# Performance work log

Hardware: AMD Instinct MI355X
Metric: run time of the kernel (lower is better)

Reference implementation:

```python
import jax, jax.numpy as jnp
import numpy as np
import math

D_MODEL = 1024
NUM_HEADS = 16
D_K = 64
B, T = 2, 2048


def setup_inputs() -> dict:
    key = jax.random.key(0)
    ks = jax.random.split(key, 12)
    s = 0.02
    return {
        "Q": jax.random.normal(ks[0], (B, T, D_MODEL), jnp.float32),
        "K": jax.random.normal(ks[1], (B, T, D_MODEL), jnp.float32),
        "V": jax.random.normal(ks[2], (B, T, D_MODEL), jnp.float32),
        # stacked per-head projection weights: [H, d_model, d_k]
        "Wq": jax.random.normal(ks[3], (NUM_HEADS, D_MODEL, D_K), jnp.float32) * s,
        "bq": jax.random.normal(ks[4], (NUM_HEADS, D_K), jnp.float32) * s,
        "Wk": jax.random.normal(ks[5], (NUM_HEADS, D_MODEL, D_K), jnp.float32) * s,
        "bk": jax.random.normal(ks[6], (NUM_HEADS, D_K), jnp.float32) * s,
        "Wv": jax.random.normal(ks[7], (NUM_HEADS, D_MODEL, D_K), jnp.float32) * s,
        "bv": jax.random.normal(ks[8], (NUM_HEADS, D_K), jnp.float32) * s,
        "Wo": jax.random.normal(ks[9], (D_MODEL, D_MODEL), jnp.float32) * s,
        "bo": jax.random.normal(ks[10], (D_MODEL,), jnp.float32) * s,
    }


def reference(Q, K, V, Wq, bq, Wk, bk, Wv, bv, Wo, bo):
    scale = 1.0 / math.sqrt(D_K)
    # fused batched per-head projections (replaces the Python per-head loop)
    Qh = jnp.einsum("btd,hdk->bhtk", Q, Wq) + bq[None, :, None, :]
    Kh = jnp.einsum("btd,hdk->bhtk", K, Wk) + bk[None, :, None, :]
    Vh = jnp.einsum("btd,hdk->bhtk", V, Wv) + bv[None, :, None, :]
    scores = jnp.einsum("bhtk,bhsk->bhts", Qh, Kh) * scale  # [B,H,T,T]
    attn = jax.nn.softmax(scores, axis=-1)
    ctx = jnp.einsum("bhts,bhsk->bhtk", attn, Vh)  # [B,H,T,d_k]
    # Faithful to the original: plain view of contiguous [B,H,T,d] into
    # [B,T,H*d] WITHOUT transposing head/time (matches torch .view semantics).
    bsz, nt = Q.shape[0], Q.shape[1]
    x = ctx.reshape(bsz, nt, NUM_HEADS * D_K)
    out = x @ Wo.T + bo
    # dropout with p=0.0 is identity; omitted for determinism
    return out
```

## Files before the change

### kernel.cpp

```cpp
#include <hip/hip_runtime.h>
#include <stdint.h>

typedef __attribute__((ext_vector_type(8))) short short8;
typedef __attribute__((ext_vector_type(4))) short short4v;
typedef __attribute__((ext_vector_type(4))) float float4v;

#define MFMA16(a, b, c) __builtin_amdgcn_mfma_f32_16x16x32_bf16((a), (b), (c), 0, 0, 0)

__device__ __forceinline__ ushort f2bf_rne(float f) {
  union { float f; unsigned u; } x; x.f = f;
  unsigned r = x.u + 0x7FFFu + ((x.u >> 16) & 1u);
  return (ushort)(r >> 16);
}
__device__ __forceinline__ ushort f2bf_trunc(float f) {
  union { float f; unsigned u; } x; x.f = f;
  return (ushort)(x.u >> 16);
}
__device__ __forceinline__ void gload16(const ushort* g, ushort* lds) {
  __builtin_amdgcn_global_load_lds(
      (__attribute__((address_space(1))) unsigned int*)g,
      (__attribute__((address_space(3))) unsigned int*)lds, 16, 0, 0);
}

#define CEXP 0.1803368801111204f

__device__ __forceinline__ void transpose64f(const float* __restrict__ in, int is,
                                             ushort* __restrict__ out, int os,
                                             ushort* lds ) {
  const int t = threadIdx.x;
#pragma unroll
  for (int it = 0; it < 2; ++it) {
    int e = it * 2048 + t * 8;
    int r = e >> 6, c = e & 63;
    const float* p = in + (size_t)r * is + c;
    float4 x0 = *(const float4*)p;
    float4 x1 = *(const float4*)(p + 4);
    ushort tv[8] __attribute__((aligned(16))) = {
        f2bf_rne(x0.x), f2bf_rne(x0.y), f2bf_rne(x0.z), f2bf_rne(x0.w),
        f2bf_rne(x1.x), f2bf_rne(x1.y), f2bf_rne(x1.z), f2bf_rne(x1.w)};
    *(uint4*)&lds[r * 72 + c] = *(const uint4*)tv;
  }
  __syncthreads();
  const int cc = t >> 2;
  const int rg = (t & 3) * 16;
  ushort tmp[16] __attribute__((aligned(16)));
#pragma unroll
  for (int i = 0; i < 16; ++i) tmp[i] = lds[(rg + i) * 72 + cc];
  *(uint4*)&out[(size_t)cc * os + rg] = *(const uint4*)&tmp[0];
  *(uint4*)&out[(size_t)cc * os + rg + 8] = *(const uint4*)&tmp[8];
}

__global__ __launch_bounds__(256) void prep_kernel(
    const float* __restrict__ Q, const float* __restrict__ K,
    const float* __restrict__ V, const float* __restrict__ Wo,
    const float* __restrict__ Wq, const float* __restrict__ Wk,
    const float* __restrict__ Wv, ushort* __restrict__ Qb, ushort* __restrict__ Kb,
    ushort* __restrict__ Vb, ushort* __restrict__ WoB, ushort* __restrict__ BtQ,
    ushort* __restrict__ BtK, ushort* __restrict__ BtV) {
  __shared__ ushort lds[64 * 72];
  const int bx = blockIdx.x;
  if (bx < 6656) {
    const float* s;
    ushort* d;
    int i;
    if (bx < 6144) {
      const int plane = bx >> 11;
      s = plane == 0 ? Q : (plane == 1 ? K : V);
      d = plane == 0 ? Qb : (plane == 1 ? Kb : Vb);
      i = ((bx & 2047) * 256 + threadIdx.x) * 8;
    } else {
      s = Wo;
      d = WoB;
      i = ((bx - 6144) * 256 + threadIdx.x) * 8;
    }
    float4 a = *(const float4*)(s + i);
    float4 b = *(const float4*)(s + i + 4);
    ushort t[8] __attribute__((aligned(16))) = {
        f2bf_rne(a.x), f2bf_rne(a.y), f2bf_rne(a.z), f2bf_rne(a.w),
        f2bf_rne(b.x), f2bf_rne(b.y), f2bf_rne(b.z), f2bf_rne(b.w)};
    *(uint4*)(d + i) = *(const uint4*)t;
  } else {
    const int rb = bx - 6656;
    const int dt = rb & 15, h = (rb >> 4) & 15, z = rb >> 8;
    const float* W = z == 0 ? Wq : (z == 1 ? Wk : Wv);
    ushort* Bt = z == 0 ? BtQ : (z == 1 ? BtK : BtV);
    transpose64f(W + h * 65536 + dt * 4096, 64, Bt + h * 65536 + dt * 64, 1024, lds);
  }
}

__global__ __launch_bounds__(256, 2) void repack_w_kernel(
    const float* __restrict__ Wq, const float* __restrict__ Wk,
    const float* __restrict__ Wv, ushort* __restrict__ BtQ, ushort* __restrict__ BtK,
    ushort* __restrict__ BtV) {
  __shared__ ushort lds[64 * 72];
  const float* W = blockIdx.z == 0 ? Wq : (blockIdx.z == 1 ? Wk : Wv);
  ushort* Bt = blockIdx.z == 0 ? BtQ : (blockIdx.z == 1 ? BtK : BtV);
  const int h = blockIdx.y, dt = blockIdx.x;
  transpose64f(W + h * 65536 + dt * 4096, 64, Bt + h * 65536 + dt * 64, 1024, lds);
}

template <int F32>
__device__ __forceinline__ void stage16(const void* G, size_t eoff, ushort* ldst) {
  if (F32) {
    const float* p = (const float*)G + eoff;
    float4 x0 = *(const float4*)p;
    float4 x1 = *(const float4*)(p + 4);
    ushort t[8] __attribute__((aligned(16))) = {
        f2bf_rne(x0.x), f2bf_rne(x0.y), f2bf_rne(x0.z), f2bf_rne(x0.w),
        f2bf_rne(x1.x), f2bf_rne(x1.y), f2bf_rne(x1.z), f2bf_rne(x1.w)};
    *(uint4*)ldst = *(const uint4*)t;
  } else {
    gload16((const ushort*)G + eoff, ldst);
  }
}

template <int AF32, int BF32>
__device__ __forceinline__ void gemm_body_basic(const void* __restrict__ A,
                                                const void* __restrict__ Bt,
                                                const float* __restrict__ bias,
                                                void* __restrict__ C, int cmode,
                                                float ascale, int N, int K, ushort* lA,
                                                ushort* lB) {
  const int tid = threadIdx.x;
  const int l = tid & 63, lane15 = l & 15, quad = l >> 4;
  const int mbase = blockIdx.y * 128, nbase = blockIdx.x * 128;
  const int w = tid >> 6;
  const int wrow = (w >> 1) * 64, wcol = (w & 1) * 64;
  const int e0 = tid * 8;
  const int e1 = 2048 + tid * 8;
  const int r0 = e0 >> 5, c0 = e0 & 31;
  const int r1 = e1 >> 5, c1 = e1 & 31;

  float4v acc[4][4];
#pragma unroll
  for (int i = 0; i < 4; ++i)
#pragma unroll
    for (int j = 0; j < 4; ++j) acc[i][j] = (float4v){0.f, 0.f, 0.f, 0.f};

  for (int kb = 0; kb < K; kb += 32) {
    __syncthreads();
    stage16<AF32>(A, (size_t)(mbase + r0) * K + c0 + kb, &lA[e0]);
    stage16<AF32>(A, (size_t)(mbase + r1) * K + c1 + kb, &lA[e1]);
    stage16<BF32>(Bt, (size_t)(nbase + r0) * K + c0 + kb, &lB[e0]);
    stage16<BF32>(Bt, (size_t)(nbase + r1) * K + c1 + kb, &lB[e1]);
    asm volatile("s_waitcnt vmcnt(0)" ::: "memory");
    __syncthreads();
    short8 a[4], b[4];
#pragma unroll
    for (int i = 0; i < 4; ++i) {
      a[i] = *(const short8*)&lA[(wrow + i * 16 + lane15) * 32 + quad * 8];
      b[i] = *(const short8*)&lB[(wcol + i * 16 + lane15) * 32 + quad * 8];
    }
#pragma unroll
    for (int i = 0; i < 4; ++i)
#pragma unroll
      for (int j = 0; j < 4; ++j) acc[i][j] = MFMA16(a[i], b[j], acc[i][j]);
  }

  if (cmode == 3) {
    __syncthreads();
    uint* sp = (uint*)lA + w * 576;
    const int bb = mbase >> 11;
    const int tb = (mbase & 2047) + wrow;
#pragma unroll
    for (int j = 0; j < 4; ++j) {
      {
        const int n = nbase + wcol + j * 16 + lane15;
        const float bvs = bias[n];
#pragma unroll
        for (int i = 0; i < 4; ++i)
#pragma unroll
          for (int rp = 0; rp < 2; ++rp) {
            const uint lo = f2bf_rne((acc[i][j][2 * rp] + bvs) * ascale);
            const uint hi = f2bf_rne((acc[i][j][2 * rp + 1] + bvs) * ascale);
            sp[36 * lane15 + i * 8 + quad * 2 + rp] = lo | (hi << 16);
          }
      }
#pragma unroll
      for (int t = 0; t < 2; ++t) {
        const int row = t * 8 + (l >> 3);
        const int c = l & 7;
        uint4 d = *(const uint4*)(sp + 36 * row + 4 * c);
        const int ng = nbase + wcol + j * 16 + row;
        ushort* dst = (ushort*)C + ((size_t)(bb * 1024 + ng)) * 2048 + tb + c * 8;
        *(uint4*)dst = d;
      }
    }
    return;
  }

#pragma unroll
  for (int j = 0; j < 4; ++j) {
    const int n = nbase + wcol + j * 16 + lane15;
    const float bvs = bias[n];
#pragma unroll
    for (int i = 0; i < 4; ++i) {
      const int m0 = mbase + wrow + i * 16 + quad * 4;
#pragma unroll
      for (int r = 0; r < 4; ++r) {
        const float val = (acc[i][j][r] + bvs) * ascale;
        if (cmode == 1) {
          const int m = m0 + r;
          const int bb = m >> 11, t = m & 2047;
          ((ushort*)C)[((size_t)(bb * 1024 + n)) * 2048 + t] = f2bf_rne(val);
        } else if (cmode == 2) {
          ((float*)C)[(size_t)(m0 + r) * N + n] = val;
        } else {
          ((ushort*)C)[(size_t)(m0 + r) * N + n] = f2bf_rne(val);
        }
      }
    }
  }
}

__global__ __launch_bounds__(256, 2) void proj3_kernel(
    const ushort* __restrict__ Qb, const ushort* __restrict__ Kb,
    const ushort* __restrict__ Vb, const ushort* __restrict__ BtQ,
    const ushort* __restrict__ BtK, const ushort* __restrict__ BtV,
    const float* __restrict__ bq, const float* __restrict__ bk,
    const float* __restrict__ bv, ushort* __restrict__ Qh, ushort* __restrict__ Kh,
    ushort* __restrict__ Vt) {
  __shared__ ushort lA[5120], lB[4096];
  if (blockIdx.z == 0)
    gemm_body_basic<0, 0>(Qb, BtQ, bq, Qh, 0, CEXP, 1024, 1024, lA, lB);
  else if (blockIdx.z == 1)
    gemm_body_basic<0, 0>(Kb, BtK, bk, Kh, 0, 1.0f, 1024, 1024, lA, lB);
  else
    gemm_body_basic<0, 0>(Vb, BtV, bv, Vt, 3, 1.0f, 1024, 1024, lA, lB);
}

__global__ __launch_bounds__(256, 2) void gemm_out_kernel(
    const ushort* __restrict__ X, const ushort* __restrict__ WoB,
    const float* __restrict__ bo, float* __restrict__ out) {
  __shared__ ushort lA[4096], lB[2048];
  const int tid = threadIdx.x;
  const int l = tid & 63, lane15 = l & 15, quad = l >> 4;
  const int mbase = blockIdx.y * 128, nbase = blockIdx.x * 64;
  const int wv = tid >> 6;
  const int wrow = wv * 32;
  const int e0 = tid * 8;
  const int e1 = 2048 + tid * 8;
  const int r0 = e0 >> 5, c0 = e0 & 31;
  const int r1 = e1 >> 5, c1 = e1 & 31;
  const ushort* Ag0 = X + (size_t)(mbase + r0) * 1024 + c0;
  const ushort* Ag1 = X + (size_t)(mbase + r1) * 1024 + c1;
  const ushort* Bg0 = WoB + (size_t)(nbase + r0) * 1024 + c0;

  float4v acc[2][4];
#pragma unroll
  for (int i = 0; i < 2; ++i)
#pragma unroll
    for (int j = 0; j < 4; ++j) acc[i][j] = (float4v){0.f, 0.f, 0.f, 0.f};

  for (int kb = 0; kb < 1024; kb += 32) {
    __syncthreads();
    gload16(Ag0 + kb, &lA[e0]);
    gload16(Ag1 + kb, &lA[e1]);
    gload16(Bg0 + kb, &lB[e0]);
    asm volatile("s_waitcnt vmcnt(0)" ::: "memory");
    __syncthreads();
    short8 a[2], b[4];
#pragma unroll
    for (int i = 0; i < 2; ++i)
      a[i] = *(const short8*)&lA[(wrow + i * 16 + lane15) * 32 + quad * 8];
#pragma unroll
    for (int j = 0; j < 4; ++j)
      b[j] = *(const short8*)&lB[(j * 16 + lane15) * 32 + quad * 8];
#pragma unroll
    for (int i = 0; i < 2; ++i)
#pragma unroll
      for (int j = 0; j < 4; ++j) acc[i][j] = MFMA16(a[i], b[j], acc[i][j]);
  }

#pragma unroll
  for (int j = 0; j < 4; ++j) {
    const int n = nbase + j * 16 + lane15;
    const float bvs = bo[n];
#pragma unroll
    for (int i = 0; i < 2; ++i) {
      const int m0 = mbase + wrow + i * 16 + quad * 4;
#pragma unroll
      for (int r = 0; r < 4; ++r) out[(size_t)(m0 + r) * 1024 + n] = acc[i][j][r] + bvs;
    }
  }
}

__global__ __launch_bounds__(256, 2) void proj3f_kernel(
    const float* __restrict__ Q, const float* __restrict__ Kin,
    const float* __restrict__ V, const ushort* __restrict__ BtQ,
    const ushort* __restrict__ BtK, const ushort* __restrict__ BtV,
    const float* __restrict__ bq, const float* __restrict__ bk,
    const float* __restrict__ bv, ushort* __restrict__ Qh, ushort* __restrict__ Kh,
    ushort* __restrict__ Vt) {
  __shared__ ushort lA[5120], lB[4096];
  if (blockIdx.z == 0)
    gemm_body_basic<1, 0>(Q, BtQ, bq, Qh, 0, CEXP, 1024, 1024, lA, lB);
  else if (blockIdx.z == 1)
    gemm_body_basic<1, 0>(Kin, BtK, bk, Kh, 0, 1.0f, 1024, 1024, lA, lB);
  else
    gemm_body_basic<1, 0>(V, BtV, bv, Vt, 3, 1.0f, 1024, 1024, lA, lB);
}

__global__ __launch_bounds__(256, 2) void gemm_btf_kernel(
    const ushort* __restrict__ X, const float* __restrict__ Wo,
    const float* __restrict__ bo, float* __restrict__ out) {
  __shared__ ushort lA[5120], lB[4096];
  gemm_body_basic<0, 1>(X, Wo, bo, out, 2, 1.0f, 1024, 1024, lA, lB);
}

__global__ __launch_bounds__(512, 4) void attn_kernel(const ushort* __restrict__ Qh,
                                                      const ushort* __restrict__ Kh,
                                                      const ushort* __restrict__ Vt,
                                                      ushort* __restrict__ ctxout) {
  __shared__ ushort lK[2][64 * 64];
  __shared__ ushort lV[2][64 * 64];
  __shared__ ushort pl_all[8][16 * 68];
  const int tid = threadIdx.x, l = tid & 63, wv = tid >> 6;
  const int lane15 = l & 15, quad = l >> 4;
  const int bh = blockIdx.x, b = bh >> 4, h = bh & 15;
  const int q0 = blockIdx.y * 128 + wv * 16;

  const int sr = tid >> 3;
  const int scb = (tid & 7) ^ (sr & 7);
  const ushort* Kp = Kh + (size_t)(b * 2048) * 1024 + h * 64;
  const ushort* Vp = Vt + (size_t)(bh * 64) * 2048;
  const ushort* Kg = Kp + (size_t)sr * 1024 + scb * 8;
  const ushort* Vg = Vp + (size_t)sr * 2048 + scb * 8;

  const ushort* qrow = Qh + (size_t)(b * 2048 + q0 + lane15) * 1024 + h * 64;
  const short8 qa0 = *(const short8*)&qrow[quad * 8];
  const short8 qa1 = *(const short8*)&qrow[32 + quad * 8];

  const int xm = lane15 & 7;
  const int fr0 = lane15 * 64 + ((quad ^ xm) * 8);
  const int fr1 = lane15 * 64 + (((quad + 4) ^ xm) * 8);

  ushort* pl = &pl_all[wv][0];
  const short8 ones = {0x3F80, 0x3F80, 0x3F80, 0x3F80, 0x3F80, 0x3F80, 0x3F80, 0x3F80};

  float4v o[4];
  float4v lf = (float4v){0.f, 0.f, 0.f, 0.f};
#pragma unroll
  for (int i = 0; i < 4; ++i) o[i] = (float4v){0.f, 0.f, 0.f, 0.f};

  gload16(Kg, &lK[0][tid * 8]);
  gload16(Vg, &lV[0][tid * 8]);
  asm volatile("s_waitcnt vmcnt(0)" ::: "memory");
  __syncthreads();

  int cur = 0;
  for (int s0 = 0; s0 < 2048; s0 += 64) {
    if (s0 + 64 < 2048) {
      gload16(Kg + (size_t)(s0 + 64) * 1024, &lK[cur ^ 1][tid * 8]);
      gload16(Vg + (s0 + 64), &lV[cur ^ 1][tid * 8]);
    }
    const ushort* Kl = &lK[cur][0];
    const ushort* Vl = &lV[cur][0];

    float4v sb[4];
    __builtin_amdgcn_s_setprio(1);
#pragma unroll
    for (int i = 0; i < 4; ++i) {
      short8 k0 = *(const short8*)&Kl[i * 1024 + fr0];
      short8 k1 = *(const short8*)&Kl[i * 1024 + fr1];
      float4v c = (float4v){0.f, 0.f, 0.f, 0.f};
      c = MFMA16(qa0, k0, c);
      c = MFMA16(qa1, k1, c);
      sb[i] = c;
    }
    __builtin_amdgcn_s_setprio(0);
#pragma unroll
    for (int i = 0; i < 4; ++i)
#pragma unroll
      for (int r = 0; r < 4; ++r)
        pl[(quad * 4 + r) * 68 + i * 16 + lane15] =
            f2bf_trunc(__builtin_amdgcn_exp2f(sb[i][r]));
    short4v p0a = *(const short4v*)&pl[lane15 * 68 + quad * 8];
    short4v p0b = *(const short4v*)&pl[lane15 * 68 + quad * 8 + 4];
    short4v p1a = *(const short4v*)&pl[lane15 * 68 + 32 + quad * 8];
    short4v p1b = *(const short4v*)&pl[lane15 * 68 + 32 + quad * 8 + 4];
    short8 pa0 = __builtin_shufflevector(p0a, p0b, 0, 1, 2, 3, 4, 5, 6, 7);
    short8 pa1 = __builtin_shufflevector(p1a, p1b, 0, 1, 2, 3, 4, 5, 6, 7);
    __builtin_amdgcn_s_setprio(1);
    lf = MFMA16(pa0, ones, lf);
    lf = MFMA16(pa1, ones, lf);
#pragma unroll
    for (int nf = 0; nf < 4; ++nf) {
      short8 v0 = *(const short8*)&Vl[nf * 1024 + fr0];
      short8 v1 = *(const short8*)&Vl[nf * 1024 + fr1];
      o[nf] = MFMA16(pa0, v0, o[nf]);
      o[nf] = MFMA16(pa1, v1, o[nf]);
    }
    __builtin_amdgcn_s_setprio(0);

    asm volatile("s_waitcnt vmcnt(0)" ::: "memory");
    __syncthreads();
    cur ^= 1;
  }

  float inv[4];
#pragma unroll
  for (int r = 0; r < 4; ++r) inv[r] = (lf[r] > 0.f) ? 1.0f / lf[r] : 0.0f;
  ushort* crow = ctxout + ((size_t)bh * 2048 + q0) * 64;
#pragma unroll
  for (int nf = 0; nf < 4; ++nf)
#pragma unroll
    for (int r = 0; r < 4; ++r)
      crow[(size_t)(quad * 4 + r) * 64 + nf * 16 + lane15] = f2bf_rne(o[nf][r] * inv[r]);
}

extern "C" void kernel_launch(void* const* d_in, const int* in_sizes, int n_in,
                              void* d_out, int out_size, void* d_ws, size_t ws_size,
                              hipStream_t stream) {
  const float* Q = (const float*)d_in[0];
  const float* K = (const float*)d_in[1];
  const float* V = (const float*)d_in[2];
  const float* Wq = (const float*)d_in[3];
  const float* bq = (const float*)d_in[4];
  const float* Wk = (const float*)d_in[5];
  const float* bk = (const float*)d_in[6];
  const float* Wv = (const float*)d_in[7];
  const float* bv = (const float*)d_in[8];
  const float* Wo = (const float*)d_in[9];
  const float* bo = (const float*)d_in[10];
  float* out = (float*)d_out;
  ushort* ws = (ushort*)d_ws;

  if (ws_size >= (58ull << 20)) {
    ushort* Qh = ws;
    ushort* Kh = Qh + (4 << 20);
    ushort* Vt = Kh + (4 << 20);
    ushort* BtQ = Vt + (4 << 20);
    ushort* BtK = BtQ + (1 << 20);
    ushort* BtV = BtK + (1 << 20);
    ushort* X = BtQ;
    ushort* WoB = ws + (16ull << 20);
    ushort* Qb = WoB + (1 << 20);
    ushort* Kb = Qb + (4 << 20);
    ushort* Vb = Kb + (4 << 20);

    prep_kernel<<<dim3(7424), 256, 0, stream>>>(Q, K, V, Wo, Wq, Wk, Wv, Qb, Kb, Vb,
                                                WoB, BtQ, BtK, BtV);
    proj3_kernel<<<dim3(8, 32, 3), 256, 0, stream>>>(Qb, Kb, Vb, BtQ, BtK, BtV, bq, bk,
                                                     bv, Qh, Kh, Vt);
    attn_kernel<<<dim3(32, 16), 512, 0, stream>>>(Qh, Kh, Vt, X);
    gemm_out_kernel<<<dim3(16, 32), 256, 0, stream>>>(X, WoB, bo, out);
  } else {
    ushort* Qh = ws;
    ushort* Kh = Qh + (4 << 20);
    ushort* Vt = Kh + (4 << 20);
    ushort* R = Vt + (4 << 20);
    ushort* BtQ = R;
    ushort* BtK = R + (1 << 20);
    ushort* BtV = R + (2 << 20);
    ushort* X = R;

    repack_w_kernel<<<dim3(16, 16, 3), 256, 0, stream>>>(Wq, Wk, Wv, BtQ, BtK, BtV);
    proj3f_kernel<<<dim3(8, 32, 3), 256, 0, stream>>>(Q, K, V, BtQ, BtK, BtV, bq, bk, bv,
                                                      Qh, Kh, Vt);
    attn_kernel<<<dim3(32, 16), 512, 0, stream>>>(Qh, Kh, Vt, X);
    gemm_btf_kernel<<<dim3(8, 32), 256, 0, stream>>>(X, Wo, bo, out);
  }
}
```

Baseline: 221.3 us.

## Keep softmax probabilities in registers via transposed QK MFMA and permlane swaps

Swaps the MFMA operand order so the score tile comes out transposed, then packs exp2 results with v_cvt_pk_bf16_f32. Lane permutes (permlane32/16 swap) rearrange them into the A-operand layout for the PV MFMA. This removes the per-wave LDS scratch buffer and its store/load round trip for P. The conversion also changes from truncation to the hardware pack instruction's rounding. Correctness depends on the permlane shuffle exactly matching the MFMA fragment layout.

```diff
diff --git a/kernel.cpp b/kernel.cpp
--- a/kernel.cpp
+++ b/kernel.cpp
@@ -314,7 +314,6 @@
                                                       ushort* __restrict__ ctxout) {
   __shared__ ushort lK[2][64 * 64];
   __shared__ ushort lV[2][64 * 64];
-  __shared__ ushort pl_all[8][16 * 68];
   const int tid = threadIdx.x, l = tid & 63, wv = tid >> 6;
   const int lane15 = l & 15, quad = l >> 4;
   const int bh = blockIdx.x, b = bh >> 4, h = bh & 15;
@@ -335,7 +334,6 @@
   const int fr0 = lane15 * 64 + ((quad ^ xm) * 8);
   const int fr1 = lane15 * 64 + (((quad + 4) ^ xm) * 8);
 
-  ushort* pl = &pl_all[wv][0];
   const short8 ones = {0x3F80, 0x3F80, 0x3F80, 0x3F80, 0x3F80, 0x3F80, 0x3F80, 0x3F80};
 
   float4v o[4];
@@ -364,23 +362,44 @@
       short8 k0 = *(const short8*)&Kl[i * 1024 + fr0];
       short8 k1 = *(const short8*)&Kl[i * 1024 + fr1];
       float4v c = (float4v){0.f, 0.f, 0.f, 0.f};
-      c = MFMA16(qa0, k0, c);
-      c = MFMA16(qa1, k1, c);
+      c = MFMA16(k0, qa0, c);
+      c = MFMA16(k1, qa1, c);
       sb[i] = c;
     }
     __builtin_amdgcn_s_setprio(0);
-#pragma unroll
-    for (int i = 0; i < 4; ++i)
-#pragma unroll
-      for (int r = 0; r < 4; ++r)
-        pl[(quad * 4 + r) * 68 + i * 16 + lane15] =
-            f2bf_trunc(__builtin_amdgcn_exp2f(sb[i][r]));
-    short4v p0a = *(const short4v*)&pl[lane15 * 68 + quad * 8];
-    short4v p0b = *(const short4v*)&pl[lane15 * 68 + quad * 8 + 4];
-    short4v p1a = *(const short4v*)&pl[lane15 * 68 + 32 + quad * 8];
-    short4v p1b = *(const short4v*)&pl[lane15 * 68 + 32 + quad * 8 + 4];
-    short8 pa0 = __builtin_shufflevector(p0a, p0b, 0, 1, 2, 3, 4, 5, 6, 7);
-    short8 pa1 = __builtin_shufflevector(p1a, p1b, 0, 1, 2, 3, 4, 5, 6, 7);
+
+    uint wpk[4][2];
+#pragma unroll
+    for (int i = 0; i < 4; ++i) {
+      const float e0 = __builtin_amdgcn_exp2f(sb[i][0]);
+      const float e1 = __builtin_amdgcn_exp2f(sb[i][1]);
+      const float e2 = __builtin_amdgcn_exp2f(sb[i][2]);
+      const float e3 = __builtin_amdgcn_exp2f(sb[i][3]);
+      asm("v_cvt_pk_bf16_f32 %0, %1, %2" : "=v"(wpk[i][0]) : "v"(e0), "v"(e1));
+      asm("v_cvt_pk_bf16_f32 %0, %1, %2" : "=v"(wpk[i][1]) : "v"(e2), "v"(e3));
+    }
+
+    union PK { uint w[4]; short8 v; };
+    PK u0, u1;
+    {
+      uint a0 = wpk[0][0], b0 = wpk[1][0];
+      asm("v_permlane32_swap_b32 %0, %1" : "+v"(a0), "+v"(b0));
+      asm("v_permlane16_swap_b32 %0, %1" : "+v"(a0), "+v"(b0));
+      uint a1 = wpk[0][1], b1 = wpk[1][1];
+      asm("v_permlane32_swap_b32 %0, %1" : "+v"(a1), "+v"(b1));
+      asm("v_permlane16_swap_b32 %0, %1" : "+v"(a1), "+v"(b1));
+      u0.w[0] = a0; u0.w[1] = a1; u0.w[2] = b0; u0.w[3] = b1;
+      uint a2 = wpk[2][0], b2 = wpk[3][0];
+      asm("v_permlane32_swap_b32 %0, %1" : "+v"(a2), "+v"(b2));
+      asm("v_permlane16_swap_b32 %0, %1" : "+v"(a2), "+v"(b2));
+      uint a3 = wpk[2][1], b3 = wpk[3][1];
+      asm("v_permlane32_swap_b32 %0, %1" : "+v"(a3), "+v"(b3));
+      asm("v_permlane16_swap_b32 %0, %1" : "+v"(a3), "+v"(b3));
+      u1.w[0] = a2; u1.w[1] = a3; u1.w[2] = b2; u1.w[3] = b3;
+    }
+    const short8 pa0 = u0.v;
+    const short8 pa1 = u1.v;
+
     __builtin_amdgcn_s_setprio(1);
     lf = MFMA16(pa0, ones, lf);
     lf = MFMA16(pa1, ones, lf);
```

New measurement: 219.2 us. Within noise of the previous version (-0.9%).
